# Optimization experiments

Measured on AMD Instinct MI355X. Metric: run time of the kernel, lower is better.

The kernel has to match this reference:

```python
import jax, jax.numpy as jnp
import numpy as np

N_EMBED = 512  # codebook size per Quantize
EPS = 1e-8


def _quantize(x, embed):
    # x: (L, d) flattened tokens; embed: (d, K) codebook
    # squared euclidean distance via expansion (as in torch source)
    dist = (x * x).sum(1, keepdims=True) - 2.0 * (x @ embed) + (embed * embed).sum(0, keepdims=True)
    ind = jnp.argmin(dist, axis=1)                      # (L,)
    q = jnp.take(embed.T, ind, axis=0)                  # (L, d) embedding lookup
    diff = jnp.mean((jax.lax.stop_gradient(q) - x) ** 2)
    q_st = x + jax.lax.stop_gradient(q - x)             # straight-through
    return q_st, diff, ind


def _ot_score(x, embed):
    # x: (L, d); embed: (d, K). OT score = sum_k (1 - cos_sim) * softmax(x@embed / K)
    xn = x / (jnp.linalg.norm(x, axis=1, keepdims=True) + EPS)
    en = embed / (jnp.linalg.norm(embed, axis=0, keepdims=True) + EPS)
    cos_dissim = jax.lax.stop_gradient(1.0 - xn @ en)   # torch version uses .data (no grad)
    cnd = jax.nn.softmax((x @ embed) * (1.0 / embed.shape[1]), axis=1)
    return (cos_dissim * cnd).sum(1)                    # (L,)


def setup_inputs() -> dict:
    key = jax.random.key(0)
    k1, k2, k3, k4 = jax.random.split(key, 4)
    n_levels, B, L, d = 5, 128, 196, 64
    input_list = jax.random.normal(k1, (n_levels, B, L, d), dtype=jnp.float32)
    cb_top = jax.random.normal(k2, (15, d, N_EMBED), dtype=jnp.float32)        # quantize_list_5
    cb_lvl = jax.random.normal(k3, (4, 15, 2 * d, N_EMBED), dtype=jnp.float32)  # quantize_list_1..4
    label = jax.random.randint(k4, (B,), 0, 15, dtype=jnp.int32)
    return {"input_list": input_list, "cb_top": cb_top, "cb_lvl": cb_lvl, "label": label}


def reference(input_list, cb_top, cb_lvl, label):
    # Hierarchical switch-VQ encode (eval mode): top level quantized with per-class
    # codebook, then each lower level concatenated with top quantized code and
    # quantized with its own per-class codebook; last level also computes OT score.
    vq = jax.vmap(_quantize)
    emb_top = cb_top[label]                              # (B, 64, 512) per-sample codebook
    q4, d4, _ = vq(input_list[4], emb_top)               # (B, L, 64)
    diff = d4.sum()
    quants, ids = [], []
    ot_score = None
    for j in (3, 2, 1, 0):                               # quantize_list_4, _3, _2, _1
        x = jnp.concatenate([input_list[j], q4], axis=-1)  # (B, L, 128)
        emb = cb_lvl[j][label]                           # (B, 128, 512)
        q, d, i = vq(x, emb)
        diff = diff + d.sum()
        quants.append(q)
        ids.append(i)
        if j == 0:                                       # OT=True level
            ot_score = jax.vmap(_ot_score)(x, emb)       # (B, L)
    quant_list = jnp.stack(quants)                       # (4, B, L, 128)
    id_list = jnp.stack(ids)                             # (4, B, L)
    return quant_list, diff, id_list, ot_score
```

## Files before the change

kernel.cpp:

```cpp
#include <hip/hip_runtime.h>
#include <hip/hip_bf16.h>
#include <math.h>

#define B 128
#define L 196
#define K 512
#define NCLS 15
#define NT 32
#define NTILES 7

#define DIFF_OFF 12845056
#define ID_OFF   12845057
#define OT_OFF   12945409

#define WS_N2   0
#define WS_INVE 38400
#define WS_PERM 46080
#define WS_LAB  46208
#define WS_CBT  46336
#define CBT_LVL 491520
#define WS_EBT_BYTES ((size_t)(46336 + 4423680) * 4)
#define EBT_LVL_BYTES 983040

#define BAND 1.0f
#define CCAP 512

typedef __attribute__((ext_vector_type(8))) short s16x8;
typedef __attribute__((ext_vector_type(4))) float f32x4;
typedef __attribute__((ext_vector_type(4))) unsigned short u16x4;

__device__ inline unsigned short f2bf(float f) {
    __hip_bfloat16 h = __float2bfloat16(f);
    return *reinterpret_cast<unsigned short*>(&h);
}

__global__ void sort_labels(const int* __restrict__ label, int* __restrict__ perm,
                            int* __restrict__ lab) {
    __shared__ int ls[B];
    const int t = threadIdx.x;
    ls[t] = label[t];
    lab[t] = ls[t];
    __syncthreads();
    const int mine = ls[t];
    int r = 0;
    for (int i = 0; i < B; ++i) {
        int li = ls[i];
        r += (li < mine) || (li == mine && i < t);
    }
    perm[r] = t;
}

__global__ __launch_bounds__(256) void precompute(
    const float* __restrict__ cb_top, const float* __restrict__ cb_lvl,
    float* __restrict__ ws)
{
    __shared__ float Ld[128][65];
    __shared__ float ps[64][4];
    const int m = blockIdx.x >> 3;
    const int c0 = (blockIdx.x & 7) * 64;
    const bool top = m < NCLS;
    const int D = top ? 64 : 128;
    const float* src = top ? cb_top + (size_t)m * 64 * K
                           : cb_lvl + (size_t)(m - NCLS) * 128 * K;
    float* cbT = ws + WS_CBT + (top ? (size_t)m * K * 64
                                    : (size_t)CBT_LVL + (size_t)(m - NCLS) * K * 128);
    unsigned short* ebt = (unsigned short*)((char*)ws + WS_EBT_BYTES +
        (top ? (size_t)m * K * 64 * 2
             : (size_t)EBT_LVL_BYTES + (size_t)(m - NCLS) * K * 128 * 2));
    const int tid = threadIdx.x;

    for (int e = tid; e < D * 64; e += 256) {
        int d = e >> 6, cc = e & 63;
        Ld[d][cc] = src[(size_t)d * K + c0 + cc];
    }
    __syncthreads();

    const int col = tid >> 2, q = tid & 3;
    const int seg = D >> 2;
    float ss = 0.f;
    for (int i = 0; i < seg; ++i) {
        int d = q * seg + i;
        float v = Ld[d][col];
        ss = fmaf(v, v, ss);
        cbT[(size_t)(c0 + col) * D + d] = v;
        ebt[(size_t)(c0 + col) * D + d] = f2bf(v);
    }
    ps[col][q] = ss;
    __syncthreads();
    if (tid < 64) {
        float n2 = (ps[tid][0] + ps[tid][1]) + (ps[tid][2] + ps[tid][3]);
        ws[WS_N2 + (size_t)m * K + c0 + tid] = n2;
        if (m >= NCLS && m < 2 * NCLS)
            ws[WS_INVE + (size_t)(m - NCLS) * K + c0 + tid] = 1.f / (sqrtf(n2) + 1e-8f);
    }
}

__global__ __launch_bounds__(256, 4) void vq_all(
    const float* __restrict__ input, float* __restrict__ ws,
    float* __restrict__ out)
{
    __shared__ float uA[NT][68];
    __shared__ float xLf[NT][68];
    __shared__ unsigned short x4_s[NT * 72];
    __shared__ unsigned short xL_s[NT * 136];
    __shared__ float clv[CCAP];
    __shared__ unsigned int clist[CCAP];
    __shared__ float wmin_s[4][NT];
    __shared__ float rowMinG[NT];
    __shared__ unsigned long long best_s[NT];
    __shared__ float xn4_s[NT], xnL_s[NT], xnq_s[NT];
    __shared__ float otZ_s[NT], otW_s[NT];
    __shared__ float dacc_s;
    __shared__ int ccnt;

    const int tid = threadIdx.x;
    const int hw = (int)blockIdx.x + 7 * (int)blockIdx.y + 896 * (int)blockIdx.z;
    const int logical = (hw & 7) * 448 + (hw >> 3);
    const int j = logical & 3;
    const int rest = logical >> 2;
    const int tile = rest % 7;
    const int ys = rest / 7;
    const int b = ((const int*)(ws + WS_PERM))[ys];
    const int cls = ((const int*)(ws + WS_LAB))[b];

    const bool OT = (j == 0);
    const bool addTop = (j == 3);
    const int t0 = tile * NT;
    const int wid = tid >> 6, lane = tid & 63, l15 = lane & 15, l4 = lane >> 4;

    const float* xin4 = input + ((size_t)(4 * B + b) * L) * 64;
    const float* xinj = input + ((size_t)(j * B + b) * L) * 64;
    const float* n2T = ws + WS_N2 + (size_t)cls * K;
    const float* n2L = ws + WS_N2 + (size_t)(NCLS + j * NCLS + cls) * K;
    const float* ive = ws + WS_INVE + (size_t)cls * K;
    const float* cbT_T = ws + WS_CBT + (size_t)cls * (K * 64);
    const float* cbT_L = ws + WS_CBT + CBT_LVL + (size_t)(j * NCLS + cls) * (K * 128);
    const unsigned short* ebT =
        (const unsigned short*)((const char*)ws + WS_EBT_BYTES) + (size_t)cls * (K * 64);
    const unsigned short* ebL =
        (const unsigned short*)((const char*)ws + WS_EBT_BYTES + EBT_LVL_BYTES) +
        (size_t)(j * NCLS + cls) * (K * 128);

    if (tid < NT) {
        xn4_s[tid] = 0.f; xnL_s[tid] = 0.f; best_s[tid] = ~0ULL;
        otZ_s[tid] = 0.f; otW_s[tid] = 0.f;
    }
    if (tid == 0) { ccnt = 0; dacc_s = 0.f; }
    __syncthreads();

    for (int idx = tid; idx < NT * 16; idx += 256) {
        int row = idx >> 4, k4 = (idx & 15) << 2;
        int l = t0 + row;
        float4 v = make_float4(0.f, 0.f, 0.f, 0.f);
        if (l < L) {
            v = *(const float4*)(xin4 + (size_t)l * 64 + k4);
            atomicAdd(&xn4_s[row], v.x * v.x + v.y * v.y + v.z * v.z + v.w * v.w);
        }
        *(float4*)&uA[row][k4] = v;
        u16x4 h; h[0] = f2bf(v.x); h[1] = f2bf(v.y); h[2] = f2bf(v.z); h[3] = f2bf(v.w);
        *(u16x4*)&x4_s[row * 72 + k4] = h;
    }
    for (int idx = tid; idx < NT * 16; idx += 256) {
        int row = idx >> 4, k4 = (idx & 15) << 2;
        int l = t0 + row;
        float4 v = make_float4(0.f, 0.f, 0.f, 0.f);
        if (l < L) {
            v = *(const float4*)(xinj + (size_t)l * 64 + k4);
            atomicAdd(&xnL_s[row], v.x * v.x + v.y * v.y + v.z * v.z + v.w * v.w);
        }
        *(float4*)&xLf[row][k4] = v;
    }
    __syncthreads();

    float runMin[2][4];
    #pragma unroll
    for (int mi = 0; mi < 2; ++mi)
        #pragma unroll
        for (int r = 0; r < 4; ++r) runMin[mi][r] = 3.4e38f;

    for (int cc = 0; cc < 2; ++cc) {
        const int colbase = cc * 256 + wid * 64;
        float n2v[4];
        #pragma unroll
        for (int ni = 0; ni < 4; ++ni) n2v[ni] = n2T[colbase + ni * 16 + l15];
        f32x4 acc[2][4] = {};
        #pragma unroll
        for (int ks = 0; ks < 2; ++ks) {
            s16x8 av[2], bv[4];
            #pragma unroll
            for (int mi = 0; mi < 2; ++mi)
                av[mi] = *(const s16x8*)&x4_s[(mi * 16 + l15) * 72 + ks * 32 + l4 * 8];
            #pragma unroll
            for (int ni = 0; ni < 4; ++ni)
                bv[ni] = *(const s16x8*)&ebT[(size_t)(colbase + ni * 16 + l15) * 64 + ks * 32 + l4 * 8];
            #pragma unroll
            for (int mi = 0; mi < 2; ++mi)
                #pragma unroll
                for (int ni = 0; ni < 4; ++ni)
                    acc[mi][ni] = __builtin_amdgcn_mfma_f32_16x16x32_bf16(
                        av[mi], bv[ni], acc[mi][ni], 0, 0, 0);
        }
        #pragma unroll
        for (int mi = 0; mi < 2; ++mi) {
            #pragma unroll
            for (int r = 0; r < 4; ++r) {
                const int row = mi * 16 + l4 * 4 + r;
                float dv[4];
                #pragma unroll
                for (int ni = 0; ni < 4; ++ni)
                    dv[ni] = n2v[ni] - 2.f * acc[mi][ni][r];
                float mnW = fminf(fminf(dv[0], dv[1]), fminf(dv[2], dv[3]));
                #pragma unroll
                for (int s = 1; s <= 8; s <<= 1)
                    mnW = fminf(mnW, __shfl_xor(mnW, s, 64));
                runMin[mi][r] = fminf(runMin[mi][r], mnW);
                const float thr = runMin[mi][r] + BAND;
                if (t0 + row < L) {
                    #pragma unroll
                    for (int ni = 0; ni < 4; ++ni) {
                        if (dv[ni] <= thr) {
                            int pos = atomicAdd(&ccnt, 1);
                            if (pos < CCAP) {
                                clist[pos] = ((unsigned)row << 16) |
                                             (unsigned)(colbase + ni * 16 + l15);
                                clv[pos] = dv[ni];
                            }
                        }
                    }
                }
            }
        }
    }
    #pragma unroll
    for (int mi = 0; mi < 2; ++mi)
        #pragma unroll
        for (int r = 0; r < 4; ++r)
            if (l15 == 0) wmin_s[wid][mi * 16 + l4 * 4 + r] = runMin[mi][r];
    __syncthreads();
    if (tid < NT)
        rowMinG[tid] = fminf(fminf(wmin_s[0][tid], wmin_s[1][tid]),
                             fminf(wmin_s[2][tid], wmin_s[3][tid]));
    __syncthreads();

    {
        const int ncand = min(ccnt, CCAP);
        const int g = tid >> 4, li = tid & 15;
        for (int e = g; e < ncand; e += 16) {
            unsigned ent = clist[e];
            int row = ent >> 16, col = ent & 0xFFFF;
            if (clv[e] > rowMinG[row] + BAND) continue;
            float4 xv = *(const float4*)&uA[row][li * 4];
            float4 ev = *(const float4*)(cbT_T + (size_t)col * 64 + li * 4);
            float prod = xv.x * ev.x + xv.y * ev.y + xv.z * ev.z + xv.w * ev.w;
            #pragma unroll
            for (int s = 1; s <= 8; s <<= 1) prod += __shfl_xor(prod, s, 64);
            if (li == 0) {
                float dvE = n2T[col] - 2.f * prod;
                unsigned u = __float_as_uint(dvE);
                u = (u & 0x80000000u) ? ~u : (u | 0x80000000u);
                atomicMin(&best_s[row], ((unsigned long long)u << 32) | (unsigned)col);
            }
        }
    }
    __syncthreads();

    {
        const int g = tid >> 4, li = tid & 15;
        #pragma unroll
        for (int rr0 = 0; rr0 < NT; rr0 += 16) {
            const int rr = rr0 + g;
            int l = t0 + rr;
            unsigned long long key = best_s[rr];
            float4 ev = make_float4(0.f, 0.f, 0.f, 0.f);
            float dvE = 0.f;
            if (l < L) {
                unsigned col = (unsigned)(key & 0xFFFFFFFFull);
                unsigned u = (unsigned)(key >> 32);
                u = (u & 0x80000000u) ? (u & 0x7FFFFFFFu) : ~u;
                dvE = __uint_as_float(u);
                ev = *(const float4*)(cbT_T + (size_t)col * 64 + li * 4);
            }
            float qs = ev.x * ev.x + ev.y * ev.y + ev.z * ev.z + ev.w * ev.w;
            #pragma unroll
            for (int s = 1; s <= 8; s <<= 1) qs += __shfl_xor(qs, s, 64);
            __syncthreads();
            *(float4*)&uA[rr][li * 4] = ev;
            u16x4 h; h[0] = f2bf(ev.x); h[1] = f2bf(ev.y); h[2] = f2bf(ev.z); h[3] = f2bf(ev.w);
            *(u16x4*)&xL_s[rr * 136 + 64 + li * 4] = h;
            if (li == 0) {
                xnq_s[rr] = qs;
                if (addTop && l < L)
                    atomicAdd(&dacc_s, (dvE + xn4_s[rr]) * (1.f / (L * 64.f)));
            }
        }
    }
    __syncthreads();

    if (tid < NT) best_s[tid] = ~0ULL;
    if (tid == 0) ccnt = 0;
    for (int idx = tid; idx < NT * 16; idx += 256) {
        int row = idx >> 4, k4 = (idx & 15) << 2;
        float4 v = *(const float4*)&xLf[row][k4];
        u16x4 h; h[0] = f2bf(v.x); h[1] = f2bf(v.y); h[2] = f2bf(v.z); h[3] = f2bf(v.w);
        *(u16x4*)&xL_s[row * 136 + k4] = h;
    }
    __syncthreads();

    #pragma unroll
    for (int mi = 0; mi < 2; ++mi)
        #pragma unroll
        for (int r = 0; r < 4; ++r) runMin[mi][r] = 3.4e38f;

    for (int cc = 0; cc < 2; ++cc) {
        const int colbase = cc * 256 + wid * 64;
        float n2v[4], iv[4];
        #pragma unroll
        for (int ni = 0; ni < 4; ++ni) {
            n2v[ni] = n2L[colbase + ni * 16 + l15];
            if (OT) iv[ni] = ive[colbase + ni * 16 + l15];
        }
        f32x4 acc[2][4] = {};
        #pragma unroll
        for (int ks = 0; ks < 4; ++ks) {
            s16x8 av[2], bv[4];
            #pragma unroll
            for (int mi = 0; mi < 2; ++mi)
                av[mi] = *(const s16x8*)&xL_s[(mi * 16 + l15) * 136 + ks * 32 + l4 * 8];
            #pragma unroll
            for (int ni = 0; ni < 4; ++ni)
                bv[ni] = *(const s16x8*)&ebL[(size_t)(colbase + ni * 16 + l15) * 128 + ks * 32 + l4 * 8];
            #pragma unroll
            for (int mi = 0; mi < 2; ++mi)
                #pragma unroll
                for (int ni = 0; ni < 4; ++ni)
                    acc[mi][ni] = __builtin_amdgcn_mfma_f32_16x16x32_bf16(
                        av[mi], bv[ni], acc[mi][ni], 0, 0, 0);
        }
        #pragma unroll
        for (int mi = 0; mi < 2; ++mi) {
            #pragma unroll
            for (int r = 0; r < 4; ++r) {
                const int row = mi * 16 + l4 * 4 + r;
                float dv[4];
                #pragma unroll
                for (int ni = 0; ni < 4; ++ni)
                    dv[ni] = n2v[ni] - 2.f * acc[mi][ni][r];
                float mnW = fminf(fminf(dv[0], dv[1]), fminf(dv[2], dv[3]));
                #pragma unroll
                for (int s = 1; s <= 8; s <<= 1)
                    mnW = fminf(mnW, __shfl_xor(mnW, s, 64));
                runMin[mi][r] = fminf(runMin[mi][r], mnW);
                const float thr = runMin[mi][r] + BAND;
                if (t0 + row < L) {
                    #pragma unroll
                    for (int ni = 0; ni < 4; ++ni) {
                        if (dv[ni] <= thr) {
                            int pos = atomicAdd(&ccnt, 1);
                            if (pos < CCAP) {
                                clist[pos] = ((unsigned)row << 16) |
                                             (unsigned)(colbase + ni * 16 + l15);
                                clv[pos] = dv[ni];
                            }
                        }
                    }
                }
                if (OT) {
                    float xn = xnL_s[row] + xnq_s[row];
                    float ivx = 1.f / (sqrtf(xn) + 1e-8f);
                    float zloc = 0.f, wloc = 0.f;
                    #pragma unroll
                    for (int ni = 0; ni < 4; ++ni) {
                        float s = acc[mi][ni][r];
                        float e = __expf(s * (1.f / 512.f));
                        zloc += e;
                        wloc += (1.f - s * ivx * iv[ni]) * e;
                    }
                    #pragma unroll
                    for (int s = 1; s <= 8; s <<= 1) {
                        zloc += __shfl_xor(zloc, s, 64);
                        wloc += __shfl_xor(wloc, s, 64);
                    }
                    if (l15 == 0) {
                        atomicAdd(&otZ_s[row], zloc);
                        atomicAdd(&otW_s[row], wloc);
                    }
                }
            }
        }
    }
    #pragma unroll
    for (int mi = 0; mi < 2; ++mi)
        #pragma unroll
        for (int r = 0; r < 4; ++r)
            if (l15 == 0) wmin_s[wid][mi * 16 + l4 * 4 + r] = runMin[mi][r];
    __syncthreads();
    if (tid < NT)
        rowMinG[tid] = fminf(fminf(wmin_s[0][tid], wmin_s[1][tid]),
                             fminf(wmin_s[2][tid], wmin_s[3][tid]));
    __syncthreads();

    {
        const int ncand = min(ccnt, CCAP);
        const int g = tid >> 4, li = tid & 15;
        for (int e = g; e < ncand; e += 16) {
            unsigned ent = clist[e];
            int row = ent >> 16, col = ent & 0xFFFF;
            if (clv[e] > rowMinG[row] + BAND) continue;
            float4 xa = *(const float4*)&xLf[row][li * 4];
            float4 xb = *(const float4*)&uA[row][li * 4];
            float4 ea = *(const float4*)(cbT_L + (size_t)col * 128 + li * 4);
            float4 eb = *(const float4*)(cbT_L + (size_t)col * 128 + 64 + li * 4);
            float prod = xa.x * ea.x + xa.y * ea.y + xa.z * ea.z + xa.w * ea.w +
                         xb.x * eb.x + xb.y * eb.y + xb.z * eb.z + xb.w * eb.w;
            #pragma unroll
            for (int s = 1; s <= 8; s <<= 1) prod += __shfl_xor(prod, s, 64);
            if (li == 0) {
                float dvE = n2L[col] - 2.f * prod;
                unsigned u = __float_as_uint(dvE);
                u = (u & 0x80000000u) ? ~u : (u | 0x80000000u);
                atomicMin(&best_s[row], ((unsigned long long)u << 32) | (unsigned)col);
            }
        }
    }
    __syncthreads();

    {
        const int slot = 3 - j;
        const int g = tid >> 4, li = tid & 15;
        for (int rr = g; rr < NT; rr += 16) {
            int l = t0 + rr;
            if (l >= L) continue;
            unsigned long long key = best_s[rr];
            unsigned col = (unsigned)(key & 0xFFFFFFFFull);
            unsigned u = (unsigned)(key >> 32);
            u = (u & 0x80000000u) ? (u & 0x7FFFFFFFu) : ~u;
            float dvE = __uint_as_float(u);
            float4 ea = *(const float4*)(cbT_L + (size_t)col * 128 + li * 4);
            float4 eb = *(const float4*)(cbT_L + (size_t)col * 128 + 64 + li * 4);
            float* dst = out + (((size_t)slot * B + b) * L + l) * 128;
            *(float4*)(dst + li * 4) = ea;
            *(float4*)(dst + 64 + li * 4) = eb;
            if (li == 0) {
                out[ID_OFF + ((size_t)slot * B + b) * L + l] = (float)col;
                if (OT) out[OT_OFF + (size_t)b * L + l] = otW_s[rr] / otZ_s[rr];
                atomicAdd(&dacc_s, (dvE + xnL_s[rr] + xnq_s[rr]) * (1.f / (L * 128.f)));
            }
        }
    }
    __syncthreads();
    if (tid == 0) atomicAdd(out + DIFF_OFF, dacc_s);
}

extern "C" void kernel_launch(void* const* d_in, const int* in_sizes, int n_in,
                              void* d_out, int out_size, void* d_ws, size_t ws_size,
                              hipStream_t stream) {
    const float* input  = (const float*)d_in[0];
    const float* cb_top = (const float*)d_in[1];
    const float* cb_lvl = (const float*)d_in[2];
    const int*   label  = (const int*)d_in[3];
    float* out = (float*)d_out;
    float* ws  = (float*)d_ws;

    hipMemsetAsync(out + DIFF_OFF, 0, sizeof(float), stream);

    sort_labels<<<1, B, 0, stream>>>(label, (int*)(ws + WS_PERM), (int*)(ws + WS_LAB));
    precompute<<<600, 256, 0, stream>>>(cb_top, cb_lvl, ws);
    vq_all<<<dim3(NTILES, B, 4), 256, 0, stream>>>(input, ws, out);
}
```

Baseline: 311.6 us.

## Fuse four VQ levels into one 512-thread block sharing top-level quantization

Each block now handles all four lower levels for one token tile, so the top-level quantization (matmul, candidate refine, lookup) is computed once per tile instead of four times. Eight waves split into four levels × two column halves for the level MFMAs, with per-level candidate lists and minima kept in shared memory. The precompute kernel also gets float4 loads and stores. In exchange, the grid shrinks fourfold, blocks get larger with more LDS, and the smaller candidate caps (128 and 256) risk overflow that would drop candidates.

```diff
diff --git a/kernel.cpp b/kernel.cpp
--- a/kernel.cpp
+++ b/kernel.cpp
@@ -7,7 +7,8 @@
 #define K 512
 #define NCLS 15
 #define NT 32
-#define NTILES 7
+#define CCT 128
+#define CCL 256
 
 #define DIFF_OFF 12845056
 #define ID_OFF   12845057
@@ -23,7 +24,6 @@
 #define EBT_LVL_BYTES 983040
 
 #define BAND 1.0f
-#define CCAP 512
 
 typedef __attribute__((ext_vector_type(8))) short s16x8;
 typedef __attribute__((ext_vector_type(4))) float f32x4;
@@ -54,7 +54,7 @@
     const float* __restrict__ cb_top, const float* __restrict__ cb_lvl,
     float* __restrict__ ws)
 {
-    __shared__ float Ld[128][65];
+    __shared__ float Ld[128][68];
     __shared__ float ps[64][4];
     const int m = blockIdx.x >> 3;
     const int c0 = (blockIdx.x & 7) * 64;
@@ -69,21 +69,25 @@
              : (size_t)EBT_LVL_BYTES + (size_t)(m - NCLS) * K * 128 * 2));
     const int tid = threadIdx.x;
 
-    for (int e = tid; e < D * 64; e += 256) {
-        int d = e >> 6, cc = e & 63;
-        Ld[d][cc] = src[(size_t)d * K + c0 + cc];
+    const int nIt = (D * 16) / 256;
+    for (int it = 0; it < nIt; ++it) {
+        int idx = it * 256 + tid;
+        int d = idx >> 4, c4 = (idx & 15) << 2;
+        *(float4*)&Ld[d][c4] = *(const float4*)(src + (size_t)d * K + c0 + c4);
     }
     __syncthreads();
 
     const int col = tid >> 2, q = tid & 3;
     const int seg = D >> 2;
     float ss = 0.f;
-    for (int i = 0; i < seg; ++i) {
+    for (int i = 0; i < seg; i += 4) {
         int d = q * seg + i;
-        float v = Ld[d][col];
-        ss = fmaf(v, v, ss);
-        cbT[(size_t)(c0 + col) * D + d] = v;
-        ebt[(size_t)(c0 + col) * D + d] = f2bf(v);
+        float4 v = make_float4(Ld[d][col], Ld[d + 1][col], Ld[d + 2][col], Ld[d + 3][col]);
+        ss = fmaf(v.x, v.x, ss); ss = fmaf(v.y, v.y, ss);
+        ss = fmaf(v.z, v.z, ss); ss = fmaf(v.w, v.w, ss);
+        *(float4*)(cbT + (size_t)(c0 + col) * D + d) = v;
+        u16x4 h; h[0] = f2bf(v.x); h[1] = f2bf(v.y); h[2] = f2bf(v.z); h[3] = f2bf(v.w);
+        *(u16x4*)(ebt + (size_t)(c0 + col) * D + d) = h;
     }
     ps[col][q] = ss;
     __syncthreads();
@@ -95,95 +99,84 @@
     }
 }
 
-__global__ __launch_bounds__(256, 4) void vq_all(
+__global__ __launch_bounds__(512, 4) void vq_all(
     const float* __restrict__ input, float* __restrict__ ws,
     float* __restrict__ out)
 {
-    __shared__ float uA[NT][68];
-    __shared__ float xLf[NT][68];
     __shared__ unsigned short x4_s[NT * 72];
-    __shared__ unsigned short xL_s[NT * 136];
-    __shared__ float clv[CCAP];
-    __shared__ unsigned int clist[CCAP];
-    __shared__ float wmin_s[4][NT];
-    __shared__ float rowMinG[NT];
-    __shared__ unsigned long long best_s[NT];
-    __shared__ float xn4_s[NT], xnL_s[NT], xnq_s[NT];
+    __shared__ unsigned short xL_s[4][NT * 136];
+    __shared__ float q4f[NT][68];
+    __shared__ float clvT[CCT];
+    __shared__ unsigned int clistT[CCT];
+    __shared__ float clvL[4][CCL];
+    __shared__ unsigned int clistL[4][CCL];
+    __shared__ float wminT[8][NT];
+    __shared__ float wminL[4][2][NT];
+    __shared__ float rowMinT[NT];
+    __shared__ float rowMinL[4][NT];
+    __shared__ unsigned long long bestT[NT];
+    __shared__ unsigned long long bestL[4][NT];
+    __shared__ float xn4_s[NT], xnq_s[NT], xnL_s[4][NT];
     __shared__ float otZ_s[NT], otW_s[NT];
+    __shared__ int ccntT, ccntL[4];
     __shared__ float dacc_s;
-    __shared__ int ccnt;
 
     const int tid = threadIdx.x;
-    const int hw = (int)blockIdx.x + 7 * (int)blockIdx.y + 896 * (int)blockIdx.z;
-    const int logical = (hw & 7) * 448 + (hw >> 3);
-    const int j = logical & 3;
-    const int rest = logical >> 2;
-    const int tile = rest % 7;
-    const int ys = rest / 7;
+    const int hw = (int)blockIdx.x + 7 * (int)blockIdx.y;
+    const int logical = (hw & 7) * 112 + (hw >> 3);
+    const int tile = logical % 7;
+    const int ys = logical / 7;
     const int b = ((const int*)(ws + WS_PERM))[ys];
     const int cls = ((const int*)(ws + WS_LAB))[b];
-
-    const bool OT = (j == 0);
-    const bool addTop = (j == 3);
     const int t0 = tile * NT;
+
     const int wid = tid >> 6, lane = tid & 63, l15 = lane & 15, l4 = lane >> 4;
+    const int g = tid >> 4, li = tid & 15;
 
     const float* xin4 = input + ((size_t)(4 * B + b) * L) * 64;
-    const float* xinj = input + ((size_t)(j * B + b) * L) * 64;
     const float* n2T = ws + WS_N2 + (size_t)cls * K;
-    const float* n2L = ws + WS_N2 + (size_t)(NCLS + j * NCLS + cls) * K;
     const float* ive = ws + WS_INVE + (size_t)cls * K;
     const float* cbT_T = ws + WS_CBT + (size_t)cls * (K * 64);
-    const float* cbT_L = ws + WS_CBT + CBT_LVL + (size_t)(j * NCLS + cls) * (K * 128);
     const unsigned short* ebT =
         (const unsigned short*)((const char*)ws + WS_EBT_BYTES) + (size_t)cls * (K * 64);
-    const unsigned short* ebL =
-        (const unsigned short*)((const char*)ws + WS_EBT_BYTES + EBT_LVL_BYTES) +
-        (size_t)(j * NCLS + cls) * (K * 128);
 
     if (tid < NT) {
-        xn4_s[tid] = 0.f; xnL_s[tid] = 0.f; best_s[tid] = ~0ULL;
+        bestT[tid] = ~0ULL;
         otZ_s[tid] = 0.f; otW_s[tid] = 0.f;
     }
-    if (tid == 0) { ccnt = 0; dacc_s = 0.f; }
-    __syncthreads();
-
-    for (int idx = tid; idx < NT * 16; idx += 256) {
-        int row = idx >> 4, k4 = (idx & 15) << 2;
-        int l = t0 + row;
-        float4 v = make_float4(0.f, 0.f, 0.f, 0.f);
-        if (l < L) {
-            v = *(const float4*)(xin4 + (size_t)l * 64 + k4);
-            atomicAdd(&xn4_s[row], v.x * v.x + v.y * v.y + v.z * v.z + v.w * v.w);
-        }
-        *(float4*)&uA[row][k4] = v;
-        u16x4 h; h[0] = f2bf(v.x); h[1] = f2bf(v.y); h[2] = f2bf(v.z); h[3] = f2bf(v.w);
-        *(u16x4*)&x4_s[row * 72 + k4] = h;
-    }
-    for (int idx = tid; idx < NT * 16; idx += 256) {
-        int row = idx >> 4, k4 = (idx & 15) << 2;
-        int l = t0 + row;
-        float4 v = make_float4(0.f, 0.f, 0.f, 0.f);
-        if (l < L) {
-            v = *(const float4*)(xinj + (size_t)l * 64 + k4);
-            atomicAdd(&xnL_s[row], v.x * v.x + v.y * v.y + v.z * v.z + v.w * v.w);
-        }
-        *(float4*)&xLf[row][k4] = v;
-    }
-    __syncthreads();
-
-    float runMin[2][4];
-    #pragma unroll
-    for (int mi = 0; mi < 2; ++mi)
-        #pragma unroll
-        for (int r = 0; r < 4; ++r) runMin[mi][r] = 3.4e38f;
-
-    for (int cc = 0; cc < 2; ++cc) {
-        const int colbase = cc * 256 + wid * 64;
-        float n2v[4];
-        #pragma unroll
-        for (int ni = 0; ni < 4; ++ni) n2v[ni] = n2T[colbase + ni * 16 + l15];
-        f32x4 acc[2][4] = {};
+    if (tid < 4 * NT) bestL[tid >> 5][tid & 31] = ~0ULL;
+    if (tid == 0) { ccntT = 0; dacc_s = 0.f; }
+    if (tid < 4) ccntL[tid] = 0;
+    __syncthreads();
+
+    {
+        const int row = g;
+        const int l = t0 + row;
+        #pragma unroll
+        for (int jj = 0; jj < 5; ++jj) {
+            const float* src = input + ((size_t)(jj * B + b) * L) * 64;
+            float4 v = make_float4(0.f, 0.f, 0.f, 0.f);
+            if (l < L) v = *(const float4*)(src + (size_t)l * 64 + li * 4);
+            float ss = v.x * v.x + v.y * v.y + v.z * v.z + v.w * v.w;
+            #pragma unroll
+            for (int s = 1; s <= 8; s <<= 1) ss += __shfl_xor(ss, s, 64);
+            u16x4 h; h[0] = f2bf(v.x); h[1] = f2bf(v.y); h[2] = f2bf(v.z); h[3] = f2bf(v.w);
+            if (jj < 4) {
+                *(u16x4*)&xL_s[jj][row * 136 + li * 4] = h;
+                if (li == 0) xnL_s[jj][row] = ss;
+            } else {
+                *(u16x4*)&x4_s[row * 72 + li * 4] = h;
+                if (li == 0) xn4_s[row] = ss;
+            }
+        }
+    }
+    __syncthreads();
+
+    f32x4 accT[2][4] = {};
+    float n2vT[4];
+    {
+        #pragma unroll
+        for (int ni = 0; ni < 4; ++ni) n2vT[ni] = n2T[wid * 64 + ni * 16 + l15];
         #pragma unroll
         for (int ks = 0; ks < 2; ++ks) {
             s16x8 av[2], bv[4];
@@ -192,64 +185,68 @@
                 av[mi] = *(const s16x8*)&x4_s[(mi * 16 + l15) * 72 + ks * 32 + l4 * 8];
             #pragma unroll
             for (int ni = 0; ni < 4; ++ni)
-                bv[ni] = *(const s16x8*)&ebT[(size_t)(colbase + ni * 16 + l15) * 64 + ks * 32 + l4 * 8];
+                bv[ni] = *(const s16x8*)&ebT[(size_t)(wid * 64 + ni * 16 + l15) * 64 + ks * 32 + l4 * 8];
             #pragma unroll
             for (int mi = 0; mi < 2; ++mi)
                 #pragma unroll
                 for (int ni = 0; ni < 4; ++ni)
-                    acc[mi][ni] = __builtin_amdgcn_mfma_f32_16x16x32_bf16(
-                        av[mi], bv[ni], acc[mi][ni], 0, 0, 0);
+                    accT[mi][ni] = __builtin_amdgcn_mfma_f32_16x16x32_bf16(
+                        av[mi], bv[ni], accT[mi][ni], 0, 0, 0);
         }
         #pragma unroll
         for (int mi = 0; mi < 2; ++mi) {
             #pragma unroll
             for (int r = 0; r < 4; ++r) {
                 const int row = mi * 16 + l4 * 4 + r;
-                float dv[4];
+                float mnW = 3.4e38f;
                 #pragma unroll
                 for (int ni = 0; ni < 4; ++ni)
-                    dv[ni] = n2v[ni] - 2.f * acc[mi][ni][r];
-                float mnW = fminf(fminf(dv[0], dv[1]), fminf(dv[2], dv[3]));
+                    mnW = fminf(mnW, n2vT[ni] - 2.f * accT[mi][ni][r]);
                 #pragma unroll
                 for (int s = 1; s <= 8; s <<= 1)
                     mnW = fminf(mnW, __shfl_xor(mnW, s, 64));
-                runMin[mi][r] = fminf(runMin[mi][r], mnW);
-                const float thr = runMin[mi][r] + BAND;
-                if (t0 + row < L) {
-                    #pragma unroll
-                    for (int ni = 0; ni < 4; ++ni) {
-                        if (dv[ni] <= thr) {
-                            int pos = atomicAdd(&ccnt, 1);
-                            if (pos < CCAP) {
-                                clist[pos] = ((unsigned)row << 16) |
-                                             (unsigned)(colbase + ni * 16 + l15);
-                                clv[pos] = dv[ni];
-                            }
-                        }
+                if (l15 == 0) wminT[wid][row] = mnW;
+            }
+        }
+    }
+    __syncthreads();
+    if (tid < NT) {
+        float mn = wminT[0][tid];
+        #pragma unroll
+        for (int w = 1; w < 8; ++w) mn = fminf(mn, wminT[w][tid]);
+        rowMinT[tid] = mn;
+    }
+    __syncthreads();
+
+    #pragma unroll
+    for (int mi = 0; mi < 2; ++mi) {
+        #pragma unroll
+        for (int r = 0; r < 4; ++r) {
+            const int row = mi * 16 + l4 * 4 + r;
+            if (t0 + row >= L) continue;
+            const float thr = rowMinT[row] + BAND;
+            #pragma unroll
+            for (int ni = 0; ni < 4; ++ni) {
+                float dv = n2vT[ni] - 2.f * accT[mi][ni][r];
+                if (dv <= thr) {
+                    int pos = atomicAdd(&ccntT, 1);
+                    if (pos < CCT) {
+                        clistT[pos] = ((unsigned)row << 16) | (unsigned)(wid * 64 + ni * 16 + l15);
+                        clvT[pos] = dv;
                     }
                 }
             }
         }
     }
-    #pragma unroll
-    for (int mi = 0; mi < 2; ++mi)
-        #pragma unroll
-        for (int r = 0; r < 4; ++r)
-            if (l15 == 0) wmin_s[wid][mi * 16 + l4 * 4 + r] = runMin[mi][r];
-    __syncthreads();
-    if (tid < NT)
-        rowMinG[tid] = fminf(fminf(wmin_s[0][tid], wmin_s[1][tid]),
-                             fminf(wmin_s[2][tid], wmin_s[3][tid]));
     __syncthreads();
 
     {
-        const int ncand = min(ccnt, CCAP);
-        const int g = tid >> 4, li = tid & 15;
-        for (int e = g; e < ncand; e += 16) {
-            unsigned ent = clist[e];
+        const int n = min(ccntT, CCT);
+        for (int e = g; e < n; e += 32) {
+            unsigned ent = clistT[e];
             int row = ent >> 16, col = ent & 0xFFFF;
-            if (clv[e] > rowMinG[row] + BAND) continue;
-            float4 xv = *(const float4*)&uA[row][li * 4];
+            int l = t0 + row;
+            float4 xv = *(const float4*)(xin4 + (size_t)l * 64 + li * 4);
             float4 ev = *(const float4*)(cbT_T + (size_t)col * 64 + li * 4);
             float prod = xv.x * ev.x + xv.y * ev.y + xv.z * ev.z + xv.w * ev.w;
             #pragma unroll
@@ -258,158 +255,173 @@
                 float dvE = n2T[col] - 2.f * prod;
                 unsigned u = __float_as_uint(dvE);
                 u = (u & 0x80000000u) ? ~u : (u | 0x80000000u);
-                atomicMin(&best_s[row], ((unsigned long long)u << 32) | (unsigned)col);
+                atomicMin(&bestT[row], ((unsigned long long)u << 32) | (unsigned)col);
             }
         }
     }
     __syncthreads();
 
     {
-        const int g = tid >> 4, li = tid & 15;
-        #pragma unroll
-        for (int rr0 = 0; rr0 < NT; rr0 += 16) {
-            const int rr = rr0 + g;
-            int l = t0 + rr;
-            unsigned long long key = best_s[rr];
-            float4 ev = make_float4(0.f, 0.f, 0.f, 0.f);
-            float dvE = 0.f;
-            if (l < L) {
-                unsigned col = (unsigned)(key & 0xFFFFFFFFull);
-                unsigned u = (unsigned)(key >> 32);
-                u = (u & 0x80000000u) ? (u & 0x7FFFFFFFu) : ~u;
-                dvE = __uint_as_float(u);
-                ev = *(const float4*)(cbT_T + (size_t)col * 64 + li * 4);
-            }
-            float qs = ev.x * ev.x + ev.y * ev.y + ev.z * ev.z + ev.w * ev.w;
-            #pragma unroll
-            for (int s = 1; s <= 8; s <<= 1) qs += __shfl_xor(qs, s, 64);
-            __syncthreads();
-            *(float4*)&uA[rr][li * 4] = ev;
-            u16x4 h; h[0] = f2bf(ev.x); h[1] = f2bf(ev.y); h[2] = f2bf(ev.z); h[3] = f2bf(ev.w);
-            *(u16x4*)&xL_s[rr * 136 + 64 + li * 4] = h;
-            if (li == 0) {
-                xnq_s[rr] = qs;
-                if (addTop && l < L)
-                    atomicAdd(&dacc_s, (dvE + xn4_s[rr]) * (1.f / (L * 64.f)));
-            }
-        }
-    }
-    __syncthreads();
-
-    if (tid < NT) best_s[tid] = ~0ULL;
-    if (tid == 0) ccnt = 0;
-    for (int idx = tid; idx < NT * 16; idx += 256) {
-        int row = idx >> 4, k4 = (idx & 15) << 2;
-        float4 v = *(const float4*)&xLf[row][k4];
-        u16x4 h; h[0] = f2bf(v.x); h[1] = f2bf(v.y); h[2] = f2bf(v.z); h[3] = f2bf(v.w);
-        *(u16x4*)&xL_s[row * 136 + k4] = h;
-    }
-    __syncthreads();
-
-    #pragma unroll
-    for (int mi = 0; mi < 2; ++mi)
-        #pragma unroll
-        for (int r = 0; r < 4; ++r) runMin[mi][r] = 3.4e38f;
-
-    for (int cc = 0; cc < 2; ++cc) {
-        const int colbase = cc * 256 + wid * 64;
-        float n2v[4], iv[4];
-        #pragma unroll
-        for (int ni = 0; ni < 4; ++ni) {
-            n2v[ni] = n2L[colbase + ni * 16 + l15];
-            if (OT) iv[ni] = ive[colbase + ni * 16 + l15];
-        }
-        f32x4 acc[2][4] = {};
-        #pragma unroll
-        for (int ks = 0; ks < 4; ++ks) {
-            s16x8 av[2], bv[4];
-            #pragma unroll
-            for (int mi = 0; mi < 2; ++mi)
-                av[mi] = *(const s16x8*)&xL_s[(mi * 16 + l15) * 136 + ks * 32 + l4 * 8];
-            #pragma unroll
-            for (int ni = 0; ni < 4; ++ni)
-                bv[ni] = *(const s16x8*)&ebL[(size_t)(colbase + ni * 16 + l15) * 128 + ks * 32 + l4 * 8];
-            #pragma unroll
-            for (int mi = 0; mi < 2; ++mi)
+        const int row = g;
+        const int l = t0 + row;
+        unsigned long long key = bestT[row];
+        float4 ev = make_float4(0.f, 0.f, 0.f, 0.f);
+        float dvE = 0.f;
+        if (l < L) {
+            unsigned col = (unsigned)(key & 0xFFFFFFFFull);
+            unsigned u = (unsigned)(key >> 32);
+            u = (u & 0x80000000u) ? (u & 0x7FFFFFFFu) : ~u;
+            dvE = __uint_as_float(u);
+            ev = *(const float4*)(cbT_T + (size_t)col * 64 + li * 4);
+        }
+        *(float4*)&q4f[row][li * 4] = ev;
+        u16x4 h; h[0] = f2bf(ev.x); h[1] = f2bf(ev.y); h[2] = f2bf(ev.z); h[3] = f2bf(ev.w);
+        #pragma unroll
+        for (int jj = 0; jj < 4; ++jj)
+            *(u16x4*)&xL_s[jj][row * 136 + 64 + li * 4] = h;
+        float qs = ev.x * ev.x + ev.y * ev.y + ev.z * ev.z + ev.w * ev.w;
+        #pragma unroll
+        for (int s = 1; s <= 8; s <<= 1) qs += __shfl_xor(qs, s, 64);
+        if (li == 0) {
+            xnq_s[row] = qs;
+            if (l < L) atomicAdd(&dacc_s, (dvE + xn4_s[row]) * (1.f / (L * 64.f)));
+        }
+    }
+    __syncthreads();
+
+    {
+        const int j = wid & 3, h = wid >> 2;
+        const bool OT = (j == 0);
+        const float* n2L = ws + WS_N2 + (size_t)(NCLS + j * NCLS + cls) * K;
+        const unsigned short* ebL =
+            (const unsigned short*)((const char*)ws + WS_EBT_BYTES + EBT_LVL_BYTES) +
+            (size_t)(j * NCLS + cls) * (K * 128);
+        const unsigned short* xj = xL_s[j];
+
+        float runMin[2][4];
+        float zS[2][4], wS[2][4];
+        #pragma unroll
+        for (int mi = 0; mi < 2; ++mi)
+            #pragma unroll
+            for (int r = 0; r < 4; ++r) {
+                runMin[mi][r] = 3.4e38f;
+                zS[mi][r] = 0.f; wS[mi][r] = 0.f;
+            }
+
+        for (int cc = 0; cc < 4; ++cc) {
+            const int colbase = h * 256 + cc * 64;
+            float n2v[4], iv[4];
+            #pragma unroll
+            for (int ni = 0; ni < 4; ++ni) {
+                n2v[ni] = n2L[colbase + ni * 16 + l15];
+                if (OT) iv[ni] = ive[colbase + ni * 16 + l15];
+            }
+            f32x4 acc[2][4] = {};
+            #pragma unroll
+            for (int ks = 0; ks < 4; ++ks) {
+                s16x8 av[2], bv[4];
+                #pragma unroll
+                for (int mi = 0; mi < 2; ++mi)
+                    av[mi] = *(const s16x8*)&xj[(mi * 16 + l15) * 136 + ks * 32 + l4 * 8];
                 #pragma unroll
                 for (int ni = 0; ni < 4; ++ni)
-                    acc[mi][ni] = __builtin_amdgcn_mfma_f32_16x16x32_bf16(
-                        av[mi], bv[ni], acc[mi][ni], 0, 0, 0);
-        }
-        #pragma unroll
-        for (int mi = 0; mi < 2; ++mi) {
-            #pragma unroll
-            for (int r = 0; r < 4; ++r) {
-                const int row = mi * 16 + l4 * 4 + r;
-                float dv[4];
-                #pragma unroll
-                for (int ni = 0; ni < 4; ++ni)
-                    dv[ni] = n2v[ni] - 2.f * acc[mi][ni][r];
-                float mnW = fminf(fminf(dv[0], dv[1]), fminf(dv[2], dv[3]));
-                #pragma unroll
-                for (int s = 1; s <= 8; s <<= 1)
-                    mnW = fminf(mnW, __shfl_xor(mnW, s, 64));
-                runMin[mi][r] = fminf(runMin[mi][r], mnW);
-                const float thr = runMin[mi][r] + BAND;
-                if (t0 + row < L) {
+                    bv[ni] = *(const s16x8*)&ebL[(size_t)(colbase + ni * 16 + l15) * 128 + ks * 32 + l4 * 8];
+                #pragma unroll
+                for (int mi = 0; mi < 2; ++mi)
                     #pragma unroll
-                    for (int ni = 0; ni < 4; ++ni) {
-                        if (dv[ni] <= thr) {
-                            int pos = atomicAdd(&ccnt, 1);
-                            if (pos < CCAP) {
-                                clist[pos] = ((unsigned)row << 16) |
-                                             (unsigned)(colbase + ni * 16 + l15);
-                                clv[pos] = dv[ni];
+                    for (int ni = 0; ni < 4; ++ni)
+                        acc[mi][ni] = __builtin_amdgcn_mfma_f32_16x16x32_bf16(
+                            av[mi], bv[ni], acc[mi][ni], 0, 0, 0);
+            }
+            #pragma unroll
+            for (int mi = 0; mi < 2; ++mi) {
+                #pragma unroll
+                for (int r = 0; r < 4; ++r) {
+                    const int row = mi * 16 + l4 * 4 + r;
+                    float dv[4];
+                    #pragma unroll
+                    for (int ni = 0; ni < 4; ++ni)
+                        dv[ni] = n2v[ni] - 2.f * acc[mi][ni][r];
+                    float mnW = fminf(fminf(dv[0], dv[1]), fminf(dv[2], dv[3]));
+                    #pragma unroll
+                    for (int s = 1; s <= 8; s <<= 1)
+                        mnW = fminf(mnW, __shfl_xor(mnW, s, 64));
+                    runMin[mi][r] = fminf(runMin[mi][r], mnW);
+                    const float thr = runMin[mi][r] + BAND;
+                    if (t0 + row < L) {
+                        #pragma unroll
+                        for (int ni = 0; ni < 4; ++ni) {
+                            if (dv[ni] <= thr) {
+                                int pos = atomicAdd(&ccntL[j], 1);
+                                if (pos < CCL) {
+                                    clistL[j][pos] = ((unsigned)row << 16) |
+                                                     (unsigned)(colbase + ni * 16 + l15);
+                                    clvL[j][pos] = dv[ni];
+                                }
                             }
                         }
                     }
+                    if (OT) {
+                        #pragma unroll
+                        for (int ni = 0; ni < 4; ++ni) {
+                            float s = acc[mi][ni][r];
+                            float e = __expf(s * (1.f / 512.f));
+                            zS[mi][r] += e;
+                            float xn = xnL_s[0][row] + xnq_s[row];
+                            float ivx = 1.f / (sqrtf(xn) + 1e-8f);
+                            wS[mi][r] += (1.f - s * ivx * iv[ni]) * e;
+                        }
+                    }
                 }
+            }
+        }
+        #pragma unroll
+        for (int mi = 0; mi < 2; ++mi)
+            #pragma unroll
+            for (int r = 0; r < 4; ++r) {
+                const int row = mi * 16 + l4 * 4 + r;
+                if (l15 == 0) wminL[j][h][row] = runMin[mi][r];
                 if (OT) {
-                    float xn = xnL_s[row] + xnq_s[row];
-                    float ivx = 1.f / (sqrtf(xn) + 1e-8f);
-                    float zloc = 0.f, wloc = 0.f;
-                    #pragma unroll
-                    for (int ni = 0; ni < 4; ++ni) {
-                        float s = acc[mi][ni][r];
-                        float e = __expf(s * (1.f / 512.f));
-                        zloc += e;
-                        wloc += (1.f - s * ivx * iv[ni]) * e;
-                    }
+                    float z = zS[mi][r], w = wS[mi][r];
                     #pragma unroll
                     for (int s = 1; s <= 8; s <<= 1) {
-                        zloc += __shfl_xor(zloc, s, 64);
-                        wloc += __shfl_xor(wloc, s, 64);
+                        z += __shfl_xor(z, s, 64);
+                        w += __shfl_xor(w, s, 64);
                     }
                     if (l15 == 0) {
-                        atomicAdd(&otZ_s[row], zloc);
-                        atomicAdd(&otW_s[row], wloc);
+                        atomicAdd(&otZ_s[row], z);
+                        atomicAdd(&otW_s[row], w);
                     }
                 }
             }
-        }
-    }
-    #pragma unroll
-    for (int mi = 0; mi < 2; ++mi)
-        #pragma unroll
-        for (int r = 0; r < 4; ++r)
-            if (l15 == 0) wmin_s[wid][mi * 16 + l4 * 4 + r] = runMin[mi][r];
-    __syncthreads();
-    if (tid < NT)
-        rowMinG[tid] = fminf(fminf(wmin_s[0][tid], wmin_s[1][tid]),
-                             fminf(wmin_s[2][tid], wmin_s[3][tid]));
-    __syncthreads();
-
-    {
-        const int ncand = min(ccnt, CCAP);
-        const int g = tid >> 4, li = tid & 15;
-        for (int e = g; e < ncand; e += 16) {
-            unsigned ent = clist[e];
+    }
+    __syncthreads();
+    if (tid < 4 * NT) {
+        int jj = tid >> 5, row = tid & 31;
+        rowMinL[jj][row] = fminf(wminL[jj][0][row], wminL[jj][1][row]);
+    }
+    __syncthreads();
+
+    for (int jj = 0; jj < 4; ++jj) {
+        const int n = min(ccntL[jj], CCL);
+        const float* xinj = input + ((size_t)(jj * B + b) * L) * 64;
+        const float* cbT_Lj = ws + WS_CBT + CBT_LVL + (size_t)(jj * NCLS + cls) * (K * 128);
+        const float* n2L = ws + WS_N2 + (size_t)(NCLS + jj * NCLS + cls) * K;
+        for (int e = g; e < n; e += 32) {
+            unsigned ent = clistL[jj][e];
             int row = ent >> 16, col = ent & 0xFFFF;
-            if (clv[e] > rowMinG[row] + BAND) continue;
-            float4 xa = *(const float4*)&xLf[row][li * 4];
-            float4 xb = *(const float4*)&uA[row][li * 4];
-            float4 ea = *(const float4*)(cbT_L + (size_t)col * 128 + li * 4);
-            float4 eb = *(const float4*)(cbT_L + (size_t)col * 128 + 64 + li * 4);
+            if (clvL[jj][e] > rowMinL[jj][row] + BAND) continue;
+            int l = t0 + row;
+            float4 xa, xb;
+            if (li < 8) {
+                xa = *(const float4*)(xinj + (size_t)l * 64 + li * 8);
+                xb = *(const float4*)(xinj + (size_t)l * 64 + li * 8 + 4);
+            } else {
+                xa = *(const float4*)&q4f[row][(li - 8) * 8];
+                xb = *(const float4*)&q4f[row][(li - 8) * 8 + 4];
+            }
+            float4 ea = *(const float4*)(cbT_Lj + (size_t)col * 128 + li * 8);
+            float4 eb = *(const float4*)(cbT_Lj + (size_t)col * 128 + li * 8 + 4);
             float prod = xa.x * ea.x + xa.y * ea.y + xa.z * ea.z + xa.w * ea.w +
                          xb.x * eb.x + xb.y * eb.y + xb.z * eb.z + xb.w * eb.w;
             #pragma unroll
@@ -418,33 +430,34 @@
                 float dvE = n2L[col] - 2.f * prod;
                 unsigned u = __float_as_uint(dvE);
                 u = (u & 0x80000000u) ? ~u : (u | 0x80000000u);
-                atomicMin(&best_s[row], ((unsigned long long)u << 32) | (unsigned)col);
-            }
-        }
-    }
-    __syncthreads();
-
-    {
-        const int slot = 3 - j;
-        const int g = tid >> 4, li = tid & 15;
-        for (int rr = g; rr < NT; rr += 16) {
-            int l = t0 + rr;
-            if (l >= L) continue;
-            unsigned long long key = best_s[rr];
-            unsigned col = (unsigned)(key & 0xFFFFFFFFull);
-            unsigned u = (unsigned)(key >> 32);
-            u = (u & 0x80000000u) ? (u & 0x7FFFFFFFu) : ~u;
-            float dvE = __uint_as_float(u);
-            float4 ea = *(const float4*)(cbT_L + (size_t)col * 128 + li * 4);
-            float4 eb = *(const float4*)(cbT_L + (size_t)col * 128 + 64 + li * 4);
-            float* dst = out + (((size_t)slot * B + b) * L + l) * 128;
-            *(float4*)(dst + li * 4) = ea;
-            *(float4*)(dst + 64 + li * 4) = eb;
-            if (li == 0) {
-                out[ID_OFF + ((size_t)slot * B + b) * L + l] = (float)col;
-                if (OT) out[OT_OFF + (size_t)b * L + l] = otW_s[rr] / otZ_s[rr];
-                atomicAdd(&dacc_s, (dvE + xnL_s[rr] + xnq_s[rr]) * (1.f / (L * 128.f)));
-            }
+                atomicMin(&bestL[jj][row], ((unsigned long long)u << 32) | (unsigned)col);
+            }
+        }
+    }
+    __syncthreads();
+
+    #pragma unroll
+    for (int it = 0; it < 4; ++it) {
+        int p = it * 32 + g;
+        int jj = p & 3, row = p >> 2;
+        int l = t0 + row;
+        if (l >= L) continue;
+        const float* cbT_Lj = ws + WS_CBT + CBT_LVL + (size_t)(jj * NCLS + cls) * (K * 128);
+        unsigned long long key = bestL[jj][row];
+        unsigned col = (unsigned)(key & 0xFFFFFFFFull);
+        unsigned u = (unsigned)(key >> 32);
+        u = (u & 0x80000000u) ? (u & 0x7FFFFFFFu) : ~u;
+        float dvE = __uint_as_float(u);
+        float4 ea = *(const float4*)(cbT_Lj + (size_t)col * 128 + li * 8);
+        float4 eb = *(const float4*)(cbT_Lj + (size_t)col * 128 + li * 8 + 4);
+        const int slot = 3 - jj;
+        float* dst = out + (((size_t)slot * B + b) * L + l) * 128 + li * 8;
+        *(float4*)dst = ea;
+        *(float4*)(dst + 4) = eb;
+        if (li == 0) {
+            out[ID_OFF + ((size_t)slot * B + b) * L + l] = (float)col;
+            if (jj == 0) out[OT_OFF + (size_t)b * L + l] = otW_s[row] / otZ_s[row];
+            atomicAdd(&dacc_s, (dvE + xnL_s[jj][row] + xnq_s[row]) * (1.f / (L * 128.f)));
         }
     }
     __syncthreads();
@@ -465,5 +478,5 @@
 
     sort_labels<<<1, B, 0, stream>>>(label, (int*)(ws + WS_PERM), (int*)(ws + WS_LAB));
     precompute<<<600, 256, 0, stream>>>(cb_top, cb_lvl, ws);
-    vq_all<<<dim3(NTILES, B, 4), 256, 0, stream>>>(input, ws, out);
+    vq_all<<<dim3(7, B), 512, 0, stream>>>(input, ws, out);
 }
```

Result: faster. 287.5 us (-7.7%).
